# Performance work log

Measured on AMD Instinct MI355X. Metric: run time of the kernel, lower is better.

## Reference

```python
import jax, jax.numpy as jnp
import numpy as np

B, S, D, H, E, K = 4, 2048, 1024, 4096, 8, 2

def setup_inputs() -> dict:
    key = jax.random.key(0)
    ks = jax.random.split(key, 7)
    scale = 0.02
    return {
        "x": jax.random.normal(ks[0], (B, S, D), dtype=jnp.float32),
        "Wg": jax.random.normal(ks[1], (D, E), dtype=jnp.float32) * scale,
        "bg": jnp.zeros((E,), dtype=jnp.float32),
        "W1": jax.random.normal(ks[2], (E, D, H), dtype=jnp.float32) * scale,
        "b1": jnp.zeros((E, H), dtype=jnp.float32),
        "W2": jax.random.normal(ks[3], (E, H, D), dtype=jnp.float32) * scale,
        "b2": jnp.zeros((E, D), dtype=jnp.float32),
    }

def reference(x, Wg, bg, W1, b1, W2, b2):
    # Gate: top-k over expert logits, softmax over the k selected logits
    logits = jnp.einsum("bsd,de->bse", x, Wg) + bg          # [B,S,E]
    topv, topi = jax.lax.top_k(logits, K)                     # [B,S,K]
    w = jax.nn.softmax(topv, axis=-1)                          # [B,S,K]
    # Combine weights per expert: sum_k w_k * one_hot(idx_k)
    combine = jnp.sum(jax.nn.one_hot(topi, E, dtype=x.dtype) * w[..., None], axis=-2)  # [B,S,E]
    # Dense per-expert FFN weighted by combine weight (zero weight -> no contribution,
    # identical math to the original masked gather/scatter formulation).
    out = jnp.zeros_like(x)
    for e in range(E):
        h = jax.nn.gelu(jnp.einsum("bsd,dh->bsh", x, W1[e]) + b1[e], approximate=False)
        y = jnp.einsum("bsh,hd->bsd", h, W2[e]) + b2[e]
        out = out + combine[..., e:e + 1] * y
    return out
```

## Files before the change

### kernel.cpp

```cpp
#include <hip/hip_runtime.h>
#include <hip/hip_bf16.h>
#include <math.h>

#define TOK   8192
#define DDIM  1024
#define HDIM  4096
#define NEXP  8
#define CAP   17408

typedef __attribute__((ext_vector_type(8))) short  bfrag;
typedef __attribute__((ext_vector_type(4))) float  ffrag;
typedef __attribute__((ext_vector_type(8))) unsigned short us8;

__device__ __forceinline__ unsigned short f2bf(float f) {
  __hip_bfloat16 b = __float2bfloat16(f);
  return *reinterpret_cast<unsigned short*>(&b);
}
__device__ __forceinline__ float bf2f(unsigned short u) {
  return __uint_as_float((unsigned int)u << 16);
}

__device__ __forceinline__ void gll16(const void* g, void* l) {
  __builtin_amdgcn_global_load_lds(
      (const __attribute__((address_space(1))) unsigned int*)g,
      (__attribute__((address_space(3))) unsigned int*)l,
      16, 0, 0);
}

__device__ __forceinline__ void local_scan(const int* __restrict__ cnt, int* offs) {
  int o = 0;
#pragma unroll
  for (int e = 0; e < NEXP; ++e) {
    offs[e] = o;
    o += ((cnt[e] + 127) >> 7) << 7;
  }
  offs[NEXP] = o;
}

__global__ __launch_bounds__(256)
void prep_kernel(const float* __restrict__ x,  const float* __restrict__ Wg,
                 const float* __restrict__ bg, unsigned short* __restrict__ xb,
                 int* __restrict__ topi, float* __restrict__ topw,
                 int* __restrict__ cnt, int* __restrict__ token_of,
                 const float* __restrict__ W1, unsigned short* __restrict__ w1b,
                 const float* __restrict__ W2, unsigned short* __restrict__ w2b) {
  __shared__ __align__(16) float T[2 * 4352];
  int tid = threadIdx.x;

  if (blockIdx.x < 256) {
    int* hist = (int*)T;
    if (tid < NEXP) hist[tid] = 0;
    int gid = blockIdx.x * 256 + tid;
    if (gid < CAP) token_of[gid] = -1;
    __syncthreads();

    int w = tid >> 6, l = tid & 63;
    const float4* wg4 = (const float4*)Wg;
#pragma unroll 1
    for (int ti = 0; ti < 8; ++ti) {
      int t = (blockIdx.x * 4 + w) * 8 + ti;
      const float4* xr = (const float4*)(x + (size_t)t * DDIM);
      float acc[8];
#pragma unroll
      for (int e = 0; e < 8; ++e) acc[e] = 0.f;
#pragma unroll
      for (int gi = 0; gi < 2; ++gi) {
        int f = gi * 128 + 2 * l;
        float4 a0 = xr[f], a1 = xr[f + 1];
        us8 o;
        o[0] = (short)f2bf(a0.x); o[1] = (short)f2bf(a0.y);
        o[2] = (short)f2bf(a0.z); o[3] = (short)f2bf(a0.w);
        o[4] = (short)f2bf(a1.x); o[5] = (short)f2bf(a1.y);
        o[6] = (short)f2bf(a1.z); o[7] = (short)f2bf(a1.w);
        *(us8*)&xb[(size_t)t * DDIM + f * 4] = o;
        float xs[8] = { a0.x, a0.y, a0.z, a0.w, a1.x, a1.y, a1.z, a1.w };
        int dbase = f * 4;
#pragma unroll
        for (int c = 0; c < 8; ++c) {
          float4 w0 = wg4[(dbase + c) * 2 + 0];
          float4 w1 = wg4[(dbase + c) * 2 + 1];
          acc[0] += xs[c] * w0.x; acc[1] += xs[c] * w0.y;
          acc[2] += xs[c] * w0.z; acc[3] += xs[c] * w0.w;
          acc[4] += xs[c] * w1.x; acc[5] += xs[c] * w1.y;
          acc[6] += xs[c] * w1.z; acc[7] += xs[c] * w1.w;
        }
      }
#pragma unroll
      for (int off = 32; off >= 1; off >>= 1)
#pragma unroll
        for (int e = 0; e < 8; ++e) acc[e] += __shfl_down(acc[e], off);
      if (l == 0) {
        float v[8];
#pragma unroll
        for (int e = 0; e < 8; ++e) v[e] = acc[e] + bg[e];
        int i0 = 0;
#pragma unroll
        for (int e = 1; e < 8; ++e) if (v[e] > v[i0]) i0 = e;
        int i1 = -1;
#pragma unroll
        for (int e = 0; e < 8; ++e) if (e != i0 && (i1 < 0 || v[e] > v[i1])) i1 = e;
        float e1 = expf(v[i1] - v[i0]);
        float s = 1.f + e1;
        topi[t * 2 + 0] = i0; topi[t * 2 + 1] = i1;
        topw[t * 2 + 0] = 1.f / s; topw[t * 2 + 1] = e1 / s;
        atomicAdd(&hist[i0], 1);
        atomicAdd(&hist[i1], 1);
      }
    }
    __syncthreads();
    if (tid < NEXP) atomicAdd(&cnt[tid], hist[tid]);
    return;
  }

  int orig = blockIdx.x - 256;
  int bid = (orig & 7) * 256 + (orig >> 3);
  const float* in; unsigned short* out; int R, C, tile;
  if (bid < 1024) { in = W1; out = w1b; R = DDIM; C = HDIM; tile = bid; }
  else            { in = W2; out = w2b; R = HDIM; C = DDIM; tile = bid - 1024; }
  int e = tile >> 7;
  int t = tile & 127;
  int tpr = C >> 8;
  int ty = t / tpr, tx = t % tpr;
  size_t bo = (size_t)e * R * C;
  in += bo; out += bo;
  int r0 = ty * 128, c0 = tx * 256;

  int r4 = (tid >> 4) * 4;
  int c4 = (tid & 15) * 4;
  int oc = tid >> 2;
  int kg = (tid & 3) * 16;

  auto ld = [&](int s, float4* v) {
    int rb = r0 + (s >> 2) * 64;
    int cb = c0 + (s & 3) * 64;
    v[0] = *(const float4*)&in[(size_t)(rb + r4 + 0) * C + cb + c4];
    v[1] = *(const float4*)&in[(size_t)(rb + r4 + 1) * C + cb + c4];
    v[2] = *(const float4*)&in[(size_t)(rb + r4 + 2) * C + cb + c4];
    v[3] = *(const float4*)&in[(size_t)(rb + r4 + 3) * C + cb + c4];
  };

  float4 v[4], nv[4];
  ld(0, v);
#pragma unroll
  for (int s = 0; s < 8; ++s) {
    if (s + 1 < 8) ld(s + 1, nv);
    float* Tb = T + (s & 1) * 4352;
    int rb = r0 + (s >> 2) * 64;
    int cb = c0 + (s & 3) * 64;
    float4 t0 = { v[0].x, v[1].x, v[2].x, v[3].x };
    float4 t1 = { v[0].y, v[1].y, v[2].y, v[3].y };
    float4 t2 = { v[0].z, v[1].z, v[2].z, v[3].z };
    float4 t3 = { v[0].w, v[1].w, v[2].w, v[3].w };
    *(float4*)&Tb[(c4 + 0) * 68 + r4] = t0;
    *(float4*)&Tb[(c4 + 1) * 68 + r4] = t1;
    *(float4*)&Tb[(c4 + 2) * 68 + r4] = t2;
    *(float4*)&Tb[(c4 + 3) * 68 + r4] = t3;
    __syncthreads();
    float4 f0 = *(const float4*)&Tb[oc * 68 + kg + 0];
    float4 f1 = *(const float4*)&Tb[oc * 68 + kg + 4];
    float4 f2 = *(const float4*)&Tb[oc * 68 + kg + 8];
    float4 f3 = *(const float4*)&Tb[oc * 68 + kg + 12];
    us8 a, b;
    a[0] = (short)f2bf(f0.x); a[1] = (short)f2bf(f0.y);
    a[2] = (short)f2bf(f0.z); a[3] = (short)f2bf(f0.w);
    a[4] = (short)f2bf(f1.x); a[5] = (short)f2bf(f1.y);
    a[6] = (short)f2bf(f1.z); a[7] = (short)f2bf(f1.w);
    b[0] = (short)f2bf(f2.x); b[1] = (short)f2bf(f2.y);
    b[2] = (short)f2bf(f2.z); b[3] = (short)f2bf(f2.w);
    b[4] = (short)f2bf(f3.x); b[5] = (short)f2bf(f3.y);
    b[6] = (short)f2bf(f3.z); b[7] = (short)f2bf(f3.w);
    size_t sub = ((size_t)(cb >> 6) * (R >> 6) + (rb >> 6)) * 4096;
    *(us8*)&out[sub + oc * 64 + kg + 0] = a;
    *(us8*)&out[sub + oc * 64 + kg + 8] = b;
    v[0] = nv[0]; v[1] = nv[1]; v[2] = nv[2]; v[3] = nv[3];
  }
}

__global__ __launch_bounds__(256) void assign_kernel(const int* __restrict__ topi,
                                                     const int* __restrict__ cnt,
                                                     int* __restrict__ cursor,
                                                     int* __restrict__ row_of,
                                                     int* __restrict__ token_of) {
  int offs[NEXP + 1];
  local_scan(cnt, offs);
  int id = blockIdx.x * 256 + threadIdx.x;
  int e = topi[id];
  int slot = atomicAdd(&cursor[e], 1);
  int row = offs[e] + slot;
  row_of[id] = row;
  token_of[row] = id >> 1;
}

template<bool INDIRECT, bool GELU, bool KSPLIT>
__global__ __launch_bounds__(256)
void moe_gemm(const unsigned short* __restrict__ A,
              const unsigned short* __restrict__ B0,
              const float* __restrict__ bias0,
              unsigned short* __restrict__ out,
              int N, int Kfull,
              const int* __restrict__ cnt,
              const int* __restrict__ token_of) {
  int offsets[NEXP + 1];
  local_scan(cnt, offsets);

  int nwg = gridDim.x * gridDim.y;
  int orig = blockIdx.y * gridDim.x + blockIdx.x;
  int V = nwg >> 3;
  int vid = (orig & 7) * V + (orig >> 3);
  int xcd = vid / V;
  int vloc = vid - xcd * V;
  int P = V / gridDim.x;
  int CW = gridDim.x >= 8 ? 8 : gridDim.x;
  int per = P * CW;
  int g = vloc / per;
  int rem = vloc - g * per;
  int m = rem / CW;
  int bx = g * CW + (rem - m * CW);
  int by = xcd * P + m;

  int kp = 0, koff = 0, Klocal = Kfull;
  if (KSPLIT) {
    kp = bx & 1; bx >>= 1;
    Klocal = Kfull >> 1;
    koff = kp * Klocal;
    out += (size_t)kp * CAP * N;
  }

  int row0 = by * 128;
  if (row0 >= offsets[NEXP]) return;
  int e = 0;
  while (row0 >= offsets[e + 1]) ++e;
  const unsigned short* B = B0 + (size_t)e * N * Kfull;
  const float* bias = bias0 + (size_t)e * N;
  int n0 = bx * 128;

  __shared__ __align__(16) char sm[49152];

  int tid = threadIdx.x;
  int w = tid >> 6, l = tid & 63;
  int lrow = l & 15, kq = l >> 4;
  int wm = w >> 1, wn = w & 1;

  int c2 = (l & 7) ^ (l >> 3);
  int rloc = ((l >> 3) << 1) + (c2 >> 2);
  int ksw = (c2 & 3) * 16;
  int s0 = 2 * w, s1 = 2 * w + 1;

  int gr0 = row0 + s0 * 16 + rloc, gr1 = row0 + s1 * 16 + rloc;
  int ar0, ar1;
  if (INDIRECT) {
    int t0 = token_of[gr0]; ar0 = t0 < 0 ? 0 : t0;
    int t1 = token_of[gr1]; ar1 = t1 < 0 ? 0 : t1;
  } else { ar0 = gr0; ar1 = gr1; }
  const char* srcA0 = (const char*)(A + (size_t)ar0 * Kfull + koff) + ksw;
  const char* srcA1 = (const char*)(A + (size_t)ar1 * Kfull + koff) + ksw;
  auto bsrc = [&](int nloc) -> const char* {
    int n = n0 + nloc;
    return (const char*)B + ((size_t)(n >> 6) * (Kfull >> 6) + (koff >> 6)) * 8192
         + (n & 63) * 128 + ksw;
  };
  const char* srcB0 = bsrc(s0 * 16 + rloc);
  const char* srcB1 = bsrc(s1 * 16 + rloc);

  auto stage = [&](int buf, int k0) {
    int kbA = k0 * 2;
    int kbB = (k0 >> 6) * 8192 + (k0 & 63) * 2;
    gll16(srcA0 + kbA, sm + buf * 8192 + s0 * 1024);
    gll16(srcA1 + kbA, sm + buf * 8192 + s1 * 1024);
    gll16(srcB0 + kbB, sm + 24576 + buf * 8192 + s0 * 1024);
    gll16(srcB1 + kbB, sm + 24576 + buf * 8192 + s1 * 1024);
  };

  int offA[4], offB[4];
#pragma unroll
  for (int i = 0; i < 4; ++i) {
    int ra = wm * 64 + i * 16 + lrow;
    offA[i] = (ra >> 1) * 128 + (((((ra & 1) << 2) + kq) ^ ((ra >> 1) & 7)) << 4);
    int rb = wn * 64 + i * 16 + lrow;
    offB[i] = 24576 + (rb >> 1) * 128 + (((((rb & 1) << 2) + kq) ^ ((rb >> 1) & 7)) << 4);
  }

  ffrag acc[4][4];
#pragma unroll
  for (int i = 0; i < 4; ++i)
#pragma unroll
    for (int j = 0; j < 4; ++j) acc[i][j] = (ffrag){0.f, 0.f, 0.f, 0.f};

  auto compute = [&](int buf) {
    int ab = buf * 8192;
    bfrag a[4], b[4];
#pragma unroll
    for (int i = 0; i < 4; ++i) a[i] = *(const bfrag*)(sm + ab + offA[i]);
#pragma unroll
    for (int j = 0; j < 4; ++j) b[j] = *(const bfrag*)(sm + ab + offB[j]);
#pragma unroll
    for (int i = 0; i < 4; ++i)
#pragma unroll
      for (int j = 0; j < 4; ++j)
        acc[i][j] = __builtin_amdgcn_mfma_f32_16x16x32_bf16(a[i], b[j], acc[i][j], 0, 0, 0);
  };

  stage(0, 0); stage(1, 32);
  asm volatile("s_waitcnt vmcnt(4)" ::: "memory");
  __builtin_amdgcn_s_barrier();

  int nk = Klocal / 32;
  int cur = 0;
  for (int kt = 0; kt < nk; ++kt) {
    int nxt2 = cur + 2; if (nxt2 >= 3) nxt2 -= 3;
    if (kt + 2 < nk) stage(nxt2, (kt + 2) * 32);
    compute(cur);
    if (kt + 1 < nk) {
      if (kt + 2 < nk) { asm volatile("s_waitcnt vmcnt(4)" ::: "memory"); }
      else             { asm volatile("s_waitcnt vmcnt(0)" ::: "memory"); }
    }
    __builtin_amdgcn_s_barrier();
    ++cur; if (cur == 3) cur = 0;
  }

  unsigned short* ht = (unsigned short*)sm;
#pragma unroll
  for (int j = 0; j < 4; ++j) {
    int col = wn * 64 + j * 16 + lrow;
    float bj = (!KSPLIT || kp == 0) ? bias[n0 + col] : 0.0f;
#pragma unroll
    for (int i = 0; i < 4; ++i) {
      int rl = wm * 64 + i * 16 + kq * 4;
#pragma unroll
      for (int r = 0; r < 4; ++r) {
        float v = acc[i][j][r] + bj;
        if (GELU) {
          float z = 1.5957691216f * (v + 0.044715f * v * v * v);
          v = v / (1.0f + __expf(-z));
        }
        ht[(rl + r) * 128 + col] = f2bf(v);
      }
    }
  }
  __syncthreads();
#pragma unroll
  for (int it = 0; it < 8; ++it) {
    int c = it * 256 + tid;
    int row = c >> 4;
    int cc = (c & 15) * 8;
    us8 v = *(const us8*)&ht[row * 128 + cc];
    *(us8*)&out[(size_t)(row0 + row) * N + n0 + cc] = v;
  }
}

__global__ __launch_bounds__(256) void combine_kernel(const unsigned short* __restrict__ y,
                                                      const int* __restrict__ row_of,
                                                      const float* __restrict__ topw,
                                                      float* __restrict__ out) {
  int t = blockIdx.x;
  int r0 = row_of[t * 2 + 0], r1 = row_of[t * 2 + 1];
  float w0 = topw[t * 2 + 0], w1 = topw[t * 2 + 1];
  const size_t P1 = (size_t)CAP * DDIM;
  const ushort4* a0 = (const ushort4*)(y + (size_t)r0 * DDIM);
  const ushort4* a1 = (const ushort4*)(y + P1 + (size_t)r0 * DDIM);
  const ushort4* b0 = (const ushort4*)(y + (size_t)r1 * DDIM);
  const ushort4* b1 = (const ushort4*)(y + P1 + (size_t)r1 * DDIM);
  float4* o = (float4*)(out + (size_t)t * DDIM);
  int i = threadIdx.x;
  ushort4 pa0 = a0[i], pa1 = a1[i], pb0 = b0[i], pb1 = b1[i];
  float4 r = {
    w0 * (bf2f(pa0.x) + bf2f(pa1.x)) + w1 * (bf2f(pb0.x) + bf2f(pb1.x)),
    w0 * (bf2f(pa0.y) + bf2f(pa1.y)) + w1 * (bf2f(pb0.y) + bf2f(pb1.y)),
    w0 * (bf2f(pa0.z) + bf2f(pa1.z)) + w1 * (bf2f(pb0.z) + bf2f(pb1.z)),
    w0 * (bf2f(pa0.w) + bf2f(pa1.w)) + w1 * (bf2f(pb0.w) + bf2f(pb1.w))
  };
  o[i] = r;
}

extern "C" void kernel_launch(void* const* d_in, const int* in_sizes, int n_in,
                              void* d_out, int out_size, void* d_ws, size_t ws_size,
                              hipStream_t stream) {
  const float* x  = (const float*)d_in[0];
  const float* Wg = (const float*)d_in[1];
  const float* bg = (const float*)d_in[2];
  const float* W1 = (const float*)d_in[3];
  const float* b1 = (const float*)d_in[4];
  const float* W2 = (const float*)d_in[5];
  const float* b2 = (const float*)d_in[6];
  float* out = (float*)d_out;

  size_t off = 0;
  char* base = (char*)d_ws;
  auto alloc = [&](size_t bytes) -> void* {
    void* p = base + off;
    off += (bytes + 255) & ~(size_t)255;
    return p;
  };
  unsigned short* xb  = (unsigned short*)alloc((size_t)TOK * DDIM * 2);
  unsigned short* w1b = (unsigned short*)alloc((size_t)NEXP * HDIM * DDIM * 2);
  unsigned short* w2b = (unsigned short*)alloc((size_t)NEXP * DDIM * HDIM * 2);
  unsigned short* h   = (unsigned short*)alloc((size_t)CAP * HDIM * 2);
  unsigned short* y   = (unsigned short*)alloc((size_t)2 * CAP * DDIM * 2);
  int*   topi     = (int*)alloc((size_t)TOK * 2 * 4);
  float* topw     = (float*)alloc((size_t)TOK * 2 * 4);
  int*   row_of   = (int*)alloc((size_t)TOK * 2 * 4);
  int*   token_of = (int*)alloc((size_t)CAP * 4);
  int*   cntcur   = (int*)alloc(64);
  if (off > ws_size) return;

  int* cnt = cntcur;
  int* cursor = cntcur + 8;

  hipMemsetAsync(cntcur, 0, 64, stream);

  prep_kernel<<<2304, 256, 0, stream>>>(x, Wg, bg, xb, topi, topw, cnt, token_of,
                                        W1, w1b, W2, w2b);
  assign_kernel<<<(TOK * 2) / 256, 256, 0, stream>>>(topi, cnt, cursor,
                                                     row_of, token_of);

  moe_gemm<true, true, false><<<dim3(HDIM / 128, CAP / 128), 256, 0, stream>>>(
      xb, w1b, b1, h, HDIM, DDIM, cnt, token_of);
  moe_gemm<false, false, true><<<dim3(16, CAP / 128), 256, 0, stream>>>(
      h, w2b, b2, y, DDIM, HDIM, cnt, token_of);

  combine_kernel<<<TOK, 256, 0, stream>>>(y, row_of, topw, out);
}
```

Before: 534.1 us.

## Drop split-K for second GEMM and switch to double-buffered LDS pipeline

```diff
diff --git a/kernel.cpp b/kernel.cpp
--- a/kernel.cpp
+++ b/kernel.cpp
@@ -191,7 +191,7 @@
   token_of[row] = id >> 1;
 }
 
-template<bool INDIRECT, bool GELU, bool KSPLIT>
+template<bool INDIRECT, bool GELU>
 __global__ __launch_bounds__(256)
 void moe_gemm(const unsigned short* __restrict__ A,
               const unsigned short* __restrict__ B0,
@@ -218,14 +218,6 @@
   int bx = g * CW + (rem - m * CW);
   int by = xcd * P + m;
 
-  int kp = 0, koff = 0, Klocal = Kfull;
-  if (KSPLIT) {
-    kp = bx & 1; bx >>= 1;
-    Klocal = Kfull >> 1;
-    koff = kp * Klocal;
-    out += (size_t)kp * CAP * N;
-  }
-
   int row0 = by * 128;
   if (row0 >= offsets[NEXP]) return;
   int e = 0;
@@ -234,7 +226,7 @@
   const float* bias = bias0 + (size_t)e * N;
   int n0 = bx * 128;
 
-  __shared__ __align__(16) char sm[49152];
+  __shared__ __align__(16) char sm[32768];
 
   int tid = threadIdx.x;
   int w = tid >> 6, l = tid & 63;
@@ -252,11 +244,11 @@
     int t0 = token_of[gr0]; ar0 = t0 < 0 ? 0 : t0;
     int t1 = token_of[gr1]; ar1 = t1 < 0 ? 0 : t1;
   } else { ar0 = gr0; ar1 = gr1; }
-  const char* srcA0 = (const char*)(A + (size_t)ar0 * Kfull + koff) + ksw;
-  const char* srcA1 = (const char*)(A + (size_t)ar1 * Kfull + koff) + ksw;
+  const char* srcA0 = (const char*)(A + (size_t)ar0 * Kfull) + ksw;
+  const char* srcA1 = (const char*)(A + (size_t)ar1 * Kfull) + ksw;
   auto bsrc = [&](int nloc) -> const char* {
     int n = n0 + nloc;
-    return (const char*)B + ((size_t)(n >> 6) * (Kfull >> 6) + (koff >> 6)) * 8192
+    return (const char*)B + ((size_t)(n >> 6) * (Kfull >> 6)) * 8192
          + (n & 63) * 128 + ksw;
   };
   const char* srcB0 = bsrc(s0 * 16 + rloc);
@@ -267,8 +259,8 @@
     int kbB = (k0 >> 6) * 8192 + (k0 & 63) * 2;
     gll16(srcA0 + kbA, sm + buf * 8192 + s0 * 1024);
     gll16(srcA1 + kbA, sm + buf * 8192 + s1 * 1024);
-    gll16(srcB0 + kbB, sm + 24576 + buf * 8192 + s0 * 1024);
-    gll16(srcB1 + kbB, sm + 24576 + buf * 8192 + s1 * 1024);
+    gll16(srcB0 + kbB, sm + 16384 + buf * 8192 + s0 * 1024);
+    gll16(srcB1 + kbB, sm + 16384 + buf * 8192 + s1 * 1024);
   };
 
   int offA[4], offB[4];
@@ -277,7 +269,7 @@
     int ra = wm * 64 + i * 16 + lrow;
     offA[i] = (ra >> 1) * 128 + (((((ra & 1) << 2) + kq) ^ ((ra >> 1) & 7)) << 4);
     int rb = wn * 64 + i * 16 + lrow;
-    offB[i] = 24576 + (rb >> 1) * 128 + (((((rb & 1) << 2) + kq) ^ ((rb >> 1) & 7)) << 4);
+    offB[i] = 16384 + (rb >> 1) * 128 + (((((rb & 1) << 2) + kq) ^ ((rb >> 1) & 7)) << 4);
   }
 
   ffrag acc[4][4];
@@ -304,25 +296,25 @@
   asm volatile("s_waitcnt vmcnt(4)" ::: "memory");
   __builtin_amdgcn_s_barrier();
 
-  int nk = Klocal / 32;
+  int nk = Kfull / 32;
   int cur = 0;
   for (int kt = 0; kt < nk; ++kt) {
-    int nxt2 = cur + 2; if (nxt2 >= 3) nxt2 -= 3;
-    if (kt + 2 < nk) stage(nxt2, (kt + 2) * 32);
     compute(cur);
+    __builtin_amdgcn_s_barrier();
+    if (kt + 2 < nk) stage(cur, (kt + 2) * 32);
     if (kt + 1 < nk) {
       if (kt + 2 < nk) { asm volatile("s_waitcnt vmcnt(4)" ::: "memory"); }
       else             { asm volatile("s_waitcnt vmcnt(0)" ::: "memory"); }
+      __builtin_amdgcn_s_barrier();
     }
-    __builtin_amdgcn_s_barrier();
-    ++cur; if (cur == 3) cur = 0;
+    cur ^= 1;
   }
 
   unsigned short* ht = (unsigned short*)sm;
 #pragma unroll
   for (int j = 0; j < 4; ++j) {
     int col = wn * 64 + j * 16 + lrow;
-    float bj = (!KSPLIT || kp == 0) ? bias[n0 + col] : 0.0f;
+    float bj = bias[n0 + col];
 #pragma unroll
     for (int i = 0; i < 4; ++i) {
       int rl = wm * 64 + i * 16 + kq * 4;
@@ -355,20 +347,13 @@
   int t = blockIdx.x;
   int r0 = row_of[t * 2 + 0], r1 = row_of[t * 2 + 1];
   float w0 = topw[t * 2 + 0], w1 = topw[t * 2 + 1];
-  const size_t P1 = (size_t)CAP * DDIM;
-  const ushort4* a0 = (const ushort4*)(y + (size_t)r0 * DDIM);
-  const ushort4* a1 = (const ushort4*)(y + P1 + (size_t)r0 * DDIM);
-  const ushort4* b0 = (const ushort4*)(y + (size_t)r1 * DDIM);
-  const ushort4* b1 = (const ushort4*)(y + P1 + (size_t)r1 * DDIM);
+  const ushort4* y0 = (const ushort4*)(y + (size_t)r0 * DDIM);
+  const ushort4* y1 = (const ushort4*)(y + (size_t)r1 * DDIM);
   float4* o = (float4*)(out + (size_t)t * DDIM);
   int i = threadIdx.x;
-  ushort4 pa0 = a0[i], pa1 = a1[i], pb0 = b0[i], pb1 = b1[i];
-  float4 r = {
-    w0 * (bf2f(pa0.x) + bf2f(pa1.x)) + w1 * (bf2f(pb0.x) + bf2f(pb1.x)),
-    w0 * (bf2f(pa0.y) + bf2f(pa1.y)) + w1 * (bf2f(pb0.y) + bf2f(pb1.y)),
-    w0 * (bf2f(pa0.z) + bf2f(pa1.z)) + w1 * (bf2f(pb0.z) + bf2f(pb1.z)),
-    w0 * (bf2f(pa0.w) + bf2f(pa1.w)) + w1 * (bf2f(pb0.w) + bf2f(pb1.w))
-  };
+  ushort4 a = y0[i], b = y1[i];
+  float4 r = { w0 * bf2f(a.x) + w1 * bf2f(b.x), w0 * bf2f(a.y) + w1 * bf2f(b.y),
+               w0 * bf2f(a.z) + w1 * bf2f(b.z), w0 * bf2f(a.w) + w1 * bf2f(b.w) };
   o[i] = r;
 }
 
@@ -395,7 +380,7 @@
   unsigned short* w1b = (unsigned short*)alloc((size_t)NEXP * HDIM * DDIM * 2);
   unsigned short* w2b = (unsigned short*)alloc((size_t)NEXP * DDIM * HDIM * 2);
   unsigned short* h   = (unsigned short*)alloc((size_t)CAP * HDIM * 2);
-  unsigned short* y   = (unsigned short*)alloc((size_t)2 * CAP * DDIM * 2);
+  unsigned short* y   = (unsigned short*)alloc((size_t)CAP * DDIM * 2);
   int*   topi     = (int*)alloc((size_t)TOK * 2 * 4);
   float* topw     = (float*)alloc((size_t)TOK * 2 * 4);
   int*   row_of   = (int*)alloc((size_t)TOK * 2 * 4);
@@ -413,9 +398,9 @@
   assign_kernel<<<(TOK * 2) / 256, 256, 0, stream>>>(topi, cnt, cursor,
                                                      row_of, token_of);
 
-  moe_gemm<true, true, false><<<dim3(HDIM / 128, CAP / 128), 256, 0, stream>>>(
+  moe_gemm<true, true><<<dim3(HDIM / 128, CAP / 128), 256, 0, stream>>>(
       xb, w1b, b1, h, HDIM, DDIM, cnt, token_of);
-  moe_gemm<false, false, true><<<dim3(16, CAP / 128), 256, 0, stream>>>(
+  moe_gemm<false, false><<<dim3(DDIM / 128, CAP / 128), 256, 0, stream>>>(
       h, w2b, b2, y, DDIM, HDIM, cnt, token_of);
 
   combine_kernel<<<TOK, 256, 0, stream>>>(y, row_of, topw, out);
```

After: 578.0 us. +8.2%, slower.
